# Kernel optimization log

Measured on AMD Instinct MI355X. Metric: run time of the kernel, lower is better.

Reference implementation:

```python
import jax, jax.numpy as jnp
import numpy as np

N_NODES = 50000
N_EDGES = 400000
N_GRAPHS = 250
D = 256
NUM_FEATURES = 256
NUM_CLASSES = 10
N_EXTRA_LAYERS = 4  # num_layers - 1
BN_EPS = 1e-5


def _mean_agg(x, src, dst, n):
    # DGL copy_u + mean over incoming edges; zero in-degree nodes get 0.
    s = jax.ops.segment_sum(x[src], dst, num_segments=n)           # [N, d]
    deg = jax.ops.segment_sum(jnp.ones((src.shape[0],), x.dtype), dst, num_segments=n)
    deg = deg[:, None]
    return jnp.where(deg > 0, s / jnp.maximum(deg, 1.0), 0.0)


def _gin_layer(x, src, dst, W1, b1, W2, b2, gamma, beta):
    n = x.shape[0]
    h = x + _mean_agg(x, src, dst, n)                              # (1+eps)*x + agg, eps=0
    h = jax.nn.relu(h @ W1 + b1) @ W2 + b2                         # apply_func MLP
    h = jax.nn.relu(h)                                             # GINConv activation
    mu = h.mean(axis=0)
    var = h.var(axis=0)                                            # biased var (torch BN train)
    return gamma * (h - mu) / jnp.sqrt(var + BN_EPS) + beta


def setup_inputs() -> dict:
    key = jax.random.key(0)
    ks = jax.random.split(key, 24)
    sc_in = 1.0 / np.sqrt(NUM_FEATURES)
    sc = 1.0 / np.sqrt(D)
    inp = {
        "x": jax.random.normal(ks[0], (N_NODES, NUM_FEATURES), dtype=jnp.float32),
        "src": jax.random.randint(ks[1], (N_EDGES,), 0, N_NODES, dtype=jnp.int32),
        "dst": jax.random.randint(ks[2], (N_EDGES,), 0, N_NODES, dtype=jnp.int32),
        "node_counts": jnp.full((N_GRAPHS,), N_NODES // N_GRAPHS, dtype=jnp.int32),
        # conv1 MLP + BN1
        "W1a": jax.random.normal(ks[3], (NUM_FEATURES, D), dtype=jnp.float32) * sc_in,
        "b1a": jnp.zeros((D,), jnp.float32),
        "W1b": jax.random.normal(ks[4], (D, D), dtype=jnp.float32) * sc,
        "b1b": jnp.zeros((D,), jnp.float32),
        "g1": jnp.ones((D,), jnp.float32),
        "be1": jnp.zeros((D,), jnp.float32),
        # stacked convs 2..5 + BNs
        "Ws1": jax.random.normal(ks[5], (N_EXTRA_LAYERS, D, D), dtype=jnp.float32) * sc,
        "bs1": jnp.zeros((N_EXTRA_LAYERS, D), jnp.float32),
        "Ws2": jax.random.normal(ks[6], (N_EXTRA_LAYERS, D, D), dtype=jnp.float32) * sc,
        "bs2": jnp.zeros((N_EXTRA_LAYERS, D), jnp.float32),
        "gammas": jnp.ones((N_EXTRA_LAYERS, D), jnp.float32),
        "betas": jnp.zeros((N_EXTRA_LAYERS, D), jnp.float32),
        # classifier
        "fcW1": jax.random.normal(ks[7], (D, D), dtype=jnp.float32) * sc,
        "fcb1": jnp.zeros((D,), jnp.float32),
        "fcW2": jax.random.normal(ks[8], (D, NUM_CLASSES), dtype=jnp.float32) * sc,
        "fcb2": jnp.zeros((NUM_CLASSES,), jnp.float32),
    }
    return inp


def reference(x, src, dst, node_counts, W1a, b1a, W1b, b1b, g1, be1,
              Ws1, bs1, Ws2, bs2, gammas, betas, fcW1, fcb1, fcW2, fcb2):
    h = _gin_layer(x, src, dst, W1a, b1a, W1b, b1b, g1, be1)
    for i in range(N_EXTRA_LAYERS):
        h = _gin_layer(h, src, dst, Ws1[i], bs1[i], Ws2[i], bs2[i], gammas[i], betas[i])
    # per-graph last-node readout
    last_idx = jnp.cumsum(node_counts) - 1                          # [n_graphs]
    g = h[last_idx]                                                 # [n_graphs, d]
    # dropout is identity in eval mode
    g = jax.nn.relu(g @ fcW1 + fcb1)
    logits = g @ fcW2 + fcb2
    return jax.nn.log_softmax(logits, axis=-1)
```

## Files before the change

kernel.cpp:

```cpp
#include <hip/hip_runtime.h>
#include <hip/hip_bf16.h>

#define N_NODESC 50000
#define N_EDGESC 400000
#define N_GRAPHSC 250
#define DDIM 256
#define NCLS 10
#define BN_EPSF 1e-5f
#define MPAD 50048
#define NBLK_GEMM 391
#define NBLK_SCAN 196

typedef __attribute__((ext_vector_type(4))) float f32x4;
typedef __attribute__((ext_vector_type(8))) short bf16x8;
typedef __attribute__((ext_vector_type(8))) unsigned short u16x8;

__device__ __forceinline__ float bf2f(unsigned short h) {
    union { unsigned int u; float f; } c;
    c.u = ((unsigned int)h) << 16;
    return c.f;
}
__device__ __forceinline__ unsigned short f2bf(float f) {
    union { float f; unsigned int u; } c;
    c.f = f;
    unsigned int u = c.u;
    return (unsigned short)((u + 0x7FFFu + ((u >> 16) & 1u)) >> 16);
}

__device__ __forceinline__ void gld_lds16(const void* g, void* l) {
    __builtin_amdgcn_global_load_lds(
        (const __attribute__((address_space(1))) unsigned int*)g,
        (__attribute__((address_space(3))) unsigned int*)l, 16, 0, 0);
}


__global__ void k_zero32(int* __restrict__ p, int n) {
    int i = blockIdx.x * blockDim.x + threadIdx.x;
    if (i < n) p[i] = 0;
}

__global__ void k_count(const int* __restrict__ dst, int* __restrict__ cnt) {
    int e = blockIdx.x * blockDim.x + threadIdx.x;
    if (e < N_EDGESC) atomicAdd(&cnt[dst[e]], 1);
}

__global__ __launch_bounds__(256) void k_scan1(const int* __restrict__ deg,
                                               int* __restrict__ rowstart,
                                               int* __restrict__ bsum) {
    __shared__ int sh[256];
    int tid = threadIdx.x;
    int i = blockIdx.x * 256 + tid;
    int v = (i < N_NODESC) ? deg[i] : 0;
    sh[tid] = v;
    __syncthreads();
    for (int off = 1; off < 256; off <<= 1) {
        int t = (tid >= off) ? sh[tid - off] : 0;
        __syncthreads();
        sh[tid] += t;
        __syncthreads();
    }
    if (i < N_NODESC) rowstart[i] = sh[tid] - v;
    if (tid == 255) bsum[blockIdx.x] = sh[255];
}

__global__ __launch_bounds__(256) void k_scan2(int* __restrict__ rowstart,
                                               const int* __restrict__ bsum) {
    __shared__ int sh[256];
    int tid = threadIdx.x;
    sh[tid] = (tid < NBLK_SCAN) ? bsum[tid] : 0;
    __syncthreads();
    for (int off = 1; off < 256; off <<= 1) {
        int t = (tid >= off) ? sh[tid - off] : 0;
        __syncthreads();
        sh[tid] += t;
        __syncthreads();
    }
    int i = blockIdx.x * 256 + tid;
    if (blockIdx.x > 0 && i < N_NODESC) rowstart[i] += sh[blockIdx.x - 1];
    if (i == 0) rowstart[N_NODESC] = N_EDGESC;
}

__global__ void k_fill(const int* __restrict__ src, const int* __restrict__ dst,
                       const int* __restrict__ rowstart, int* __restrict__ cur,
                       int* __restrict__ esrc) {
    int e = blockIdx.x * blockDim.x + threadIdx.x;
    if (e < N_EDGESC) {
        int d = dst[e];
        int pos = rowstart[d] + atomicAdd(&cur[d], 1);
        esrc[pos] = src[e];
    }
}


__global__ __launch_bounds__(256) void k_wprep(const float* __restrict__ W1a,
                                               const float* __restrict__ W1b,
                                               const float* __restrict__ Ws1,
                                               const float* __restrict__ Ws2,
                                               unsigned short* __restrict__ Wt) {
    int i = blockIdx.x * blockDim.x + threadIdx.x;
    if (i >= 10 * 65536) return;
    int m = i >> 16;
    int r = i & 65535;
    int n = r >> 8;
    int k = r & 255;
    int l = m >> 1, wsel = m & 1;
    const float* src = (l == 0) ? (wsel ? W1b : W1a)
                                : (wsel ? Ws2 + (size_t)(l - 1) * 65536
                                        : Ws1 + (size_t)(l - 1) * 65536);
    Wt[i] = f2bf(src[(size_t)k * 256 + n]);
}

__global__ __launch_bounds__(256) void k_xbf(const float* __restrict__ X,
                                             unsigned short* __restrict__ Y) {
    int i = blockIdx.x * 256 + threadIdx.x;
    if (i < N_NODESC * 64) {
        float4 v = ((const float4*)X)[i];
        ushort4 o;
        o.x = f2bf(v.x); o.y = f2bf(v.y); o.z = f2bf(v.z); o.w = f2bf(v.w);
        ((ushort4*)Y)[i] = o;
    }
}


__global__ __launch_bounds__(256) void k_agg_bf(const unsigned short* __restrict__ X,
                                                const int* __restrict__ esrc,
                                                const int* __restrict__ rowstart,
                                                const float* __restrict__ stat,
                                                const float* __restrict__ gamma,
                                                const float* __restrict__ beta,
                                                unsigned short* __restrict__ Hout) {
    int node = blockIdx.x * 8 + (threadIdx.x >> 5);
    if (node >= N_NODESC) return;
    int lane = threadIdx.x & 31;
    int d0 = lane * 8;
    float sc[8], tt[8];
    if (stat) {
        const float invN = 1.0f / (float)N_NODESC;
#pragma unroll
        for (int q = 0; q < 8; q++) {
            float mu = stat[d0 + q] * invN;
            float var = stat[256 + d0 + q] * invN - mu * mu;
            float s = gamma[d0 + q] * rsqrtf(var + BN_EPSF);
            sc[q] = s;
            tt[q] = beta[d0 + q] - s * mu;
        }
    } else {
#pragma unroll
        for (int q = 0; q < 8; q++) { sc[q] = 1.f; tt[q] = 0.f; }
    }
    int beg = rowstart[node];
    int end = rowstart[node + 1];
    float s0[8], s1[8], s2[8], s3[8];
#pragma unroll
    for (int q = 0; q < 8; q++) { s0[q] = 0.f; s1[q] = 0.f; s2[q] = 0.f; s3[q] = 0.f; }
    int j = beg;
    for (; j + 4 <= end; j += 4) {
        int sn0 = esrc[j], sn1 = esrc[j + 1], sn2 = esrc[j + 2], sn3 = esrc[j + 3];
        u16x8 v0 = *(const u16x8*)(X + (size_t)sn0 * DDIM + d0);
        u16x8 v1 = *(const u16x8*)(X + (size_t)sn1 * DDIM + d0);
        u16x8 v2 = *(const u16x8*)(X + (size_t)sn2 * DDIM + d0);
        u16x8 v3 = *(const u16x8*)(X + (size_t)sn3 * DDIM + d0);
#pragma unroll
        for (int q = 0; q < 8; q++) {
            s0[q] += bf2f(v0[q]);
            s1[q] += bf2f(v1[q]);
            s2[q] += bf2f(v2[q]);
            s3[q] += bf2f(v3[q]);
        }
    }
    for (; j < end; j++) {
        int sn0 = esrc[j];
        u16x8 v0 = *(const u16x8*)(X + (size_t)sn0 * DDIM + d0);
#pragma unroll
        for (int q = 0; q < 8; q++) s0[q] += bf2f(v0[q]);
    }
    float inv = (end > beg) ? 1.0f / (float)(end - beg) : 0.0f;
    float cnt = (end > beg) ? 2.0f : 1.0f;
    u16x8 xv = *(const u16x8*)(X + (size_t)node * DDIM + d0);
    u16x8 o;
#pragma unroll
    for (int q = 0; q < 8; q++) {
        float s = s0[q] + s1[q] + s2[q] + s3[q];
        o[q] = f2bf(sc[q] * (bf2f(xv[q]) + s * inv) + tt[q] * cnt);
    }
    *(u16x8*)(Hout + (size_t)node * DDIM + d0) = o;
}


__global__ __launch_bounds__(256) void k_gemm(const unsigned short* __restrict__ A,
                                              const unsigned short* __restrict__ Wt,
                                              const float* __restrict__ bias,
                                              unsigned short* __restrict__ C,
                                              float* __restrict__ part) {
    __shared__ unsigned short As[128 * 32];
    __shared__ unsigned short Bs[128 * 32];
    __shared__ unsigned short Ct[128 * 128];
    __shared__ float sred[2][256];

    const int tid = threadIdx.x;
    const int wv = tid >> 6;
    const int lane = tid & 63;
    const int bm = blockIdx.x;
    const int bn = blockIdx.y;

    const int wr = (wv >> 1) * 64;
    const int wc = (wv & 1) * 64;
    const int lr = lane & 15;
    const int lk = lane >> 4;

    f32x4 acc[4][4];
#pragma unroll
    for (int m = 0; m < 4; m++)
#pragma unroll
        for (int n = 0; n < 4; n++) acc[m][n] = (f32x4)(0.f);

    for (int k0 = 0; k0 < 256; k0 += 32) {
#pragma unroll
        for (int i = 0; i < 2; i++) {
            int c = wv * 128 + i * 64 + lane;
            int row = c >> 2;
            int kc = (c & 3) ^ ((row >> 1) & 3);
            const unsigned short* ga = A + (size_t)(bm * 128 + row) * 256 + k0 + kc * 8;
            gld_lds16(ga, (void*)&As[(size_t)(wv * 128 + i * 64) * 8]);
            const unsigned short* gb = Wt + (size_t)(bn * 128 + row) * 256 + k0 + kc * 8;
            gld_lds16(gb, (void*)&Bs[(size_t)(wv * 128 + i * 64) * 8]);
        }
        __syncthreads();

        bf16x8 af[4], bfr[4];
#pragma unroll
        for (int m = 0; m < 4; m++) {
            int row = wr + m * 16 + lr;
            af[m] = ((const bf16x8*)As)[row * 4 + (lk ^ ((row >> 1) & 3))];
        }
#pragma unroll
        for (int n = 0; n < 4; n++) {
            int row = wc + n * 16 + lr;
            bfr[n] = ((const bf16x8*)Bs)[row * 4 + (lk ^ ((row >> 1) & 3))];
        }
#pragma unroll
        for (int m = 0; m < 4; m++)
#pragma unroll
            for (int n = 0; n < 4; n++)
                acc[m][n] = __builtin_amdgcn_mfma_f32_16x16x32_bf16(af[m], bfr[n],
                                                                    acc[m][n], 0, 0, 0);
        __syncthreads();
    }

#pragma unroll
    for (int n = 0; n < 4; n++) {
        int cloc = wc + n * 16 + lr;
        float bv = bias[bn * 128 + cloc];
        float sp = 0.f, ssp = 0.f;
#pragma unroll
        for (int m = 0; m < 4; m++)
#pragma unroll
            for (int i = 0; i < 4; i++) {
                int row = wr + m * 16 + lk * 4 + i;
                float v = fmaxf(acc[m][n][i] + bv, 0.f);
                Ct[row * 128 + (((cloc >> 3) ^ (row & 7)) << 3) + (cloc & 7)] = f2bf(v);
                if (bm * 128 + row < N_NODESC) { sp += v; ssp += v * v; }
            }
        if (part) {
            sp += __shfl_xor(sp, 16);
            sp += __shfl_xor(sp, 32);
            ssp += __shfl_xor(ssp, 16);
            ssp += __shfl_xor(ssp, 32);
            if (lane < 16) {
                sred[wv >> 1][cloc] = sp;
                sred[wv >> 1][128 + cloc] = ssp;
            }
        }
    }
    __syncthreads();

#pragma unroll
    for (int it = 0; it < 8; it++) {
        int chunk = it * 256 + tid;
        int row = chunk >> 4;
        int cc = chunk & 15;
        u16x8 v = *(const u16x8*)&Ct[row * 128 + ((cc ^ (row & 7)) << 3)];
        *(u16x8*)(C + (size_t)(bm * 128 + row) * DDIM + bn * 128 + cc * 8) = v;
    }
    if (part && tid < 256) {
        float v = sred[0][tid] + sred[1][tid];
        int cloc = tid & 127;
        int off = (tid < 128) ? (bn * 128 + cloc) : (256 + bn * 128 + cloc);
        part[(size_t)bm * 512 + off] = v;
    }
}


__global__ __launch_bounds__(512) void k_statred1(const float* __restrict__ part,
                                                  float* __restrict__ part2) {
    int t = threadIdx.x;
    int b0 = blockIdx.x * 17;
    float s = 0.f;
#pragma unroll 4
    for (int j = 0; j < 17; j++) s += part[(size_t)(b0 + j) * 512 + t];
    part2[(size_t)blockIdx.x * 512 + t] = s;
}

__global__ __launch_bounds__(512) void k_statred2(const float* __restrict__ part2,
                                                  float* __restrict__ stat) {
    int t = threadIdx.x;
    float s = 0.f;
#pragma unroll 4
    for (int j = 0; j < 23; j++) s += part2[(size_t)j * 512 + t];
    stat[t] = s;
}


__global__ __launch_bounds__(256) void k_head(const unsigned short* __restrict__ Y,
                                              const int* __restrict__ counts,
                                              const float* __restrict__ stat,
                                              const float* __restrict__ gamma,
                                              const float* __restrict__ beta,
                                              const float* __restrict__ fcW1,
                                              const float* __restrict__ fcb1,
                                              const float* __restrict__ fcW2,
                                              const float* __restrict__ fcb2,
                                              float* __restrict__ out) {
    int g = blockIdx.x;
    __shared__ float row[DDIM];
    __shared__ float gv[DDIM];
    __shared__ float logits[NCLS];
    __shared__ int lastIdx;
    if (threadIdx.x == 0) {
        int s = 0;
        for (int i = 0; i <= g; i++) s += counts[i];
        lastIdx = s - 1;
    }
    __syncthreads();
    int j = threadIdx.x;
    const float invN = 1.0f / (float)N_NODESC;
    float mu = stat[j] * invN;
    float var = stat[256 + j] * invN - mu * mu;
    float sc = gamma[j] * rsqrtf(var + BN_EPSF);
    row[j] = sc * (bf2f(Y[(size_t)lastIdx * DDIM + j]) - mu) + beta[j];
    __syncthreads();
    float acc = fcb1[j];
    for (int d = 0; d < DDIM; d++) acc += row[d] * fcW1[(size_t)d * DDIM + j];
    gv[j] = fmaxf(acc, 0.f);
    __syncthreads();
    if (j < NCLS) {
        float a = fcb2[j];
        for (int d = 0; d < DDIM; d++) a += gv[d] * fcW2[(size_t)d * NCLS + j];
        logits[j] = a;
    }
    __syncthreads();
    if (j == 0) {
        float m = -1e30f;
        for (int c = 0; c < NCLS; c++) m = fmaxf(m, logits[c]);
        float se = 0.f;
        for (int c = 0; c < NCLS; c++) se += expf(logits[c] - m);
        float lse = m + logf(se);
        for (int c = 0; c < NCLS; c++) out[g * NCLS + c] = logits[c] - lse;
    }
}


extern "C" void kernel_launch(void* const* d_in, const int* in_sizes, int n_in,
                              void* d_out, int out_size, void* d_ws, size_t ws_size,
                              hipStream_t stream) {
    const float* x    = (const float*)d_in[0];
    const int* src    = (const int*)d_in[1];
    const int* dst    = (const int*)d_in[2];
    const int* counts = (const int*)d_in[3];
    const float* W1a  = (const float*)d_in[4];
    const float* b1a  = (const float*)d_in[5];
    const float* W1b  = (const float*)d_in[6];
    const float* b1b  = (const float*)d_in[7];
    const float* g1   = (const float*)d_in[8];
    const float* be1  = (const float*)d_in[9];
    const float* Ws1  = (const float*)d_in[10];
    const float* bs1  = (const float*)d_in[11];
    const float* Ws2  = (const float*)d_in[12];
    const float* bs2  = (const float*)d_in[13];
    const float* gms  = (const float*)d_in[14];
    const float* bts  = (const float*)d_in[15];
    const float* fcW1 = (const float*)d_in[16];
    const float* fcb1 = (const float*)d_in[17];
    const float* fcW2 = (const float*)d_in[18];
    const float* fcb2 = (const float*)d_in[19];
    float* out = (float*)d_out;

    char* ws = (char*)d_ws;
    const size_t BUF = (size_t)MPAD * DDIM * 2;
    unsigned short* B0 = (unsigned short*)(ws);
    unsigned short* B1 = (unsigned short*)(ws + BUF);
    unsigned short* B2 = (unsigned short*)(ws + 2 * BUF);
    unsigned short* Bx = (unsigned short*)(ws + 3 * BUF);
    unsigned short* Wt = (unsigned short*)(ws + 4 * BUF);
    int* rowstart      = (int*)(ws + 4 * BUF + 1310720);
    int* cursor        = (int*)(ws + 4 * BUF + 1510784);
    int* esrc          = (int*)(ws + 4 * BUF + 1710848);
    float* stats       = (float*)(ws + 4 * BUF + 3310848);
    int* bsum          = (int*)(ws + 4 * BUF + 3321088);
    float* stats_part  = (float*)(ws + 4 * BUF + 3321872 + 16);
    float* stats_part2 = (float*)(ws + 4 * BUF + 4122656 + 32);

    k_zero32<<<dim3((N_NODESC + 255) / 256), 256, 0, stream>>>(cursor, N_NODESC);
    k_count<<<dim3((N_EDGESC + 255) / 256), 256, 0, stream>>>(dst, cursor);
    k_scan1<<<dim3(NBLK_SCAN), 256, 0, stream>>>(cursor, rowstart, bsum);
    k_scan2<<<dim3(NBLK_SCAN), 256, 0, stream>>>(rowstart, bsum);
    k_zero32<<<dim3((N_NODESC + 255) / 256), 256, 0, stream>>>(cursor, N_NODESC);
    k_fill<<<dim3((N_EDGESC + 255) / 256), 256, 0, stream>>>(src, dst, rowstart,
                                                             cursor, esrc);

    k_wprep<<<dim3((10 * 65536 + 255) / 256), 256, 0, stream>>>(W1a, W1b, Ws1, Ws2, Wt);
    k_xbf<<<dim3(12500), 256, 0, stream>>>(x, Bx);

    for (int l = 0; l < 5; ++l) {
        const float* B1b = (l == 0) ? b1a : bs1 + (l - 1) * 256;
        const float* B2b = (l == 0) ? b1b : bs2 + (l - 1) * 256;
        const unsigned short* Wt1 = Wt + (size_t)(l * 2) * 65536;
        const unsigned short* Wt2 = Wt + (size_t)(l * 2 + 1) * 65536;

        if (l == 0) {
            k_agg_bf<<<dim3(6250), 256, 0, stream>>>(Bx, esrc, rowstart, nullptr,
                                                     nullptr, nullptr, B1);
        } else {
            const float* GA = (l == 1) ? g1 : gms + (l - 2) * 256;
            const float* BE = (l == 1) ? be1 : bts + (l - 2) * 256;
            k_agg_bf<<<dim3(6250), 256, 0, stream>>>(B0, esrc, rowstart,
                                                     stats + (size_t)(l - 1) * 512,
                                                     GA, BE, B1);
        }
        k_gemm<<<dim3(NBLK_GEMM, 2), 256, 0, stream>>>(B1, Wt1, B1b, B2, nullptr);
        k_gemm<<<dim3(NBLK_GEMM, 2), 256, 0, stream>>>(B2, Wt2, B2b, B0, stats_part);
        k_statred1<<<dim3(23), 512, 0, stream>>>(stats_part, stats_part2);
        k_statred2<<<dim3(1), 512, 0, stream>>>(stats_part2,
                                                stats + (size_t)l * 512);
    }

    k_head<<<dim3(N_GRAPHSC), 256, 0, stream>>>(B0, counts, stats + 4 * 512,
                                                gms + 3 * 256, bts + 3 * 256,
                                                fcW1, fcb1, fcW2, fcb2, out);
}
```

Measured before the change: 538.7 us.

## Widen GEMM block tile to full 256 output columns per block

Each GEMM block now computes a 128x256 output tile instead of 128x128, so the grid drops its second dimension and every A tile is loaded from global memory once instead of twice. Each wave holds 4x8 accumulator fragments and the epilogue writes the two column halves in sequence through the shared staging buffer. Per-column BN partial sums are collected for all 256 columns in one block. In exchange, register and LDS use per block go up, and the grid is half as large, which may lower occupancy and parallelism on the GPU.

```diff
diff --git a/kernel.cpp b/kernel.cpp
--- a/kernel.cpp
+++ b/kernel.cpp
@@ -193,26 +193,26 @@
                                               unsigned short* __restrict__ C,
                                               float* __restrict__ part) {
     __shared__ unsigned short As[128 * 32];
-    __shared__ unsigned short Bs[128 * 32];
+    __shared__ unsigned short Bs[256 * 32];
     __shared__ unsigned short Ct[128 * 128];
-    __shared__ float sred[2][256];
+    __shared__ float sred[2][512];
 
     const int tid = threadIdx.x;
     const int wv = tid >> 6;
     const int lane = tid & 63;
     const int bm = blockIdx.x;
-    const int bn = blockIdx.y;
 
     const int wr = (wv >> 1) * 64;
-    const int wc = (wv & 1) * 64;
+    const int wch = wv & 1;
+    const int wc = wch * 128;
     const int lr = lane & 15;
     const int lk = lane >> 4;
 
-    f32x4 acc[4][4];
+    f32x4 acc[4][8];
 #pragma unroll
     for (int m = 0; m < 4; m++)
 #pragma unroll
-        for (int n = 0; n < 4; n++) acc[m][n] = (f32x4)(0.f);
+        for (int n = 0; n < 8; n++) acc[m][n] = (f32x4)(0.f);
 
     for (int k0 = 0; k0 < 256; k0 += 32) {
 #pragma unroll
@@ -220,73 +220,84 @@
             int c = wv * 128 + i * 64 + lane;
             int row = c >> 2;
             int kc = (c & 3) ^ ((row >> 1) & 3);
-            const unsigned short* ga = A + (size_t)(bm * 128 + row) * 256 + k0 + kc * 8;
-            gld_lds16(ga, (void*)&As[(size_t)(wv * 128 + i * 64) * 8]);
-            const unsigned short* gb = Wt + (size_t)(bn * 128 + row) * 256 + k0 + kc * 8;
-            gld_lds16(gb, (void*)&Bs[(size_t)(wv * 128 + i * 64) * 8]);
-        }
-        __syncthreads();
-
-        bf16x8 af[4], bfr[4];
+            gld_lds16(A + (size_t)(bm * 128 + row) * 256 + k0 + kc * 8,
+                      (void*)&As[(size_t)(wv * 128 + i * 64) * 8]);
+        }
+#pragma unroll
+        for (int i = 0; i < 4; i++) {
+            int c = wv * 256 + i * 64 + lane;
+            int row = c >> 2;
+            int kc = (c & 3) ^ ((row >> 1) & 3);
+            gld_lds16(Wt + (size_t)row * 256 + k0 + kc * 8,
+                      (void*)&Bs[(size_t)(wv * 256 + i * 64) * 8]);
+        }
+        __syncthreads();
+
+        bf16x8 af[4], bfr[8];
 #pragma unroll
         for (int m = 0; m < 4; m++) {
             int row = wr + m * 16 + lr;
             af[m] = ((const bf16x8*)As)[row * 4 + (lk ^ ((row >> 1) & 3))];
         }
 #pragma unroll
-        for (int n = 0; n < 4; n++) {
+        for (int n = 0; n < 8; n++) {
             int row = wc + n * 16 + lr;
             bfr[n] = ((const bf16x8*)Bs)[row * 4 + (lk ^ ((row >> 1) & 3))];
         }
 #pragma unroll
         for (int m = 0; m < 4; m++)
 #pragma unroll
-            for (int n = 0; n < 4; n++)
+            for (int n = 0; n < 8; n++)
                 acc[m][n] = __builtin_amdgcn_mfma_f32_16x16x32_bf16(af[m], bfr[n],
                                                                     acc[m][n], 0, 0, 0);
         __syncthreads();
     }
 
-#pragma unroll
-    for (int n = 0; n < 4; n++) {
-        int cloc = wc + n * 16 + lr;
-        float bv = bias[bn * 128 + cloc];
-        float sp = 0.f, ssp = 0.f;
-#pragma unroll
-        for (int m = 0; m < 4; m++)
-#pragma unroll
-            for (int i = 0; i < 4; i++) {
-                int row = wr + m * 16 + lk * 4 + i;
-                float v = fmaxf(acc[m][n][i] + bv, 0.f);
-                Ct[row * 128 + (((cloc >> 3) ^ (row & 7)) << 3) + (cloc & 7)] = f2bf(v);
-                if (bm * 128 + row < N_NODESC) { sp += v; ssp += v * v; }
+    for (int h = 0; h < 2; h++) {
+        if (wch == h) {
+#pragma unroll
+            for (int n = 0; n < 8; n++) {
+                int cl = n * 16 + lr;
+                int colg = h * 128 + cl;
+                float bv = bias[colg];
+                float sp = 0.f, ssp = 0.f;
+#pragma unroll
+                for (int m = 0; m < 4; m++)
+#pragma unroll
+                    for (int i = 0; i < 4; i++) {
+                        int row = wr + m * 16 + lk * 4 + i;
+                        float v = fmaxf(acc[m][n][i] + bv, 0.f);
+                        Ct[row * 128 + (((cl >> 3) ^ (row & 7)) << 3) + (cl & 7)] =
+                            f2bf(v);
+                        if (bm * 128 + row < N_NODESC) { sp += v; ssp += v * v; }
+                    }
+                if (part) {
+                    sp += __shfl_xor(sp, 16);
+                    sp += __shfl_xor(sp, 32);
+                    ssp += __shfl_xor(ssp, 16);
+                    ssp += __shfl_xor(ssp, 32);
+                    if (lane < 16) {
+                        sred[wv >> 1][colg] = sp;
+                        sred[wv >> 1][256 + colg] = ssp;
+                    }
+                }
             }
-        if (part) {
-            sp += __shfl_xor(sp, 16);
-            sp += __shfl_xor(sp, 32);
-            ssp += __shfl_xor(ssp, 16);
-            ssp += __shfl_xor(ssp, 32);
-            if (lane < 16) {
-                sred[wv >> 1][cloc] = sp;
-                sred[wv >> 1][128 + cloc] = ssp;
-            }
-        }
-    }
-    __syncthreads();
-
-#pragma unroll
-    for (int it = 0; it < 8; it++) {
-        int chunk = it * 256 + tid;
-        int row = chunk >> 4;
-        int cc = chunk & 15;
-        u16x8 v = *(const u16x8*)&Ct[row * 128 + ((cc ^ (row & 7)) << 3)];
-        *(u16x8*)(C + (size_t)(bm * 128 + row) * DDIM + bn * 128 + cc * 8) = v;
-    }
-    if (part && tid < 256) {
-        float v = sred[0][tid] + sred[1][tid];
-        int cloc = tid & 127;
-        int off = (tid < 128) ? (bn * 128 + cloc) : (256 + bn * 128 + cloc);
-        part[(size_t)bm * 512 + off] = v;
+        }
+        __syncthreads();
+#pragma unroll
+        for (int it = 0; it < 8; it++) {
+            int chunk = it * 256 + tid;
+            int row = chunk >> 4;
+            int cc = chunk & 15;
+            u16x8 v = *(const u16x8*)&Ct[row * 128 + ((cc ^ (row & 7)) << 3)];
+            *(u16x8*)(C + (size_t)(bm * 128 + row) * DDIM + h * 128 + cc * 8) = v;
+        }
+        __syncthreads();
+    }
+
+    if (part) {
+        part[(size_t)bm * 512 + tid] = sred[0][tid] + sred[1][tid];
+        part[(size_t)bm * 512 + 256 + tid] = sred[0][256 + tid] + sred[1][256 + tid];
     }
 }
 
@@ -427,8 +438,8 @@
                                                      stats + (size_t)(l - 1) * 512,
                                                      GA, BE, B1);
         }
-        k_gemm<<<dim3(NBLK_GEMM, 2), 256, 0, stream>>>(B1, Wt1, B1b, B2, nullptr);
-        k_gemm<<<dim3(NBLK_GEMM, 2), 256, 0, stream>>>(B2, Wt2, B2b, B0, stats_part);
+        k_gemm<<<dim3(NBLK_GEMM), 256, 0, stream>>>(B1, Wt1, B1b, B2, nullptr);
+        k_gemm<<<dim3(NBLK_GEMM), 256, 0, stream>>>(B2, Wt2, B2b, B0, stats_part);
         k_statred1<<<dim3(23), 512, 0, stream>>>(stats_part, stats_part2);
         k_statred2<<<dim3(1), 512, 0, stream>>>(stats_part2,
                                                 stats + (size_t)l * 512);
```

Result: slower. 707.6 us (+31.3%).
